# Kernel optimization log

Measured on AMD Instinct MI355X. Metric: run time of the kernel, lower is better.

## Reference

```python
import jax, jax.numpy as jnp
import numpy as np
import math

D_MODEL = 256
N_HEADS = 8
NUM_NODES = 20
KSIZE = 3
EPS = 1e-5


def _ln(x, g, b):
    m = jnp.mean(x, axis=-1, keepdims=True)
    v = jnp.mean(jnp.square(x - m), axis=-1, keepdims=True)
    return (x - m) * jax.lax.rsqrt(v + EPS) * g + b


def _conv1d(x_bdn, w_oik):
    # x: [B, D, N], w: [O, I, K], SAME padding, no bias
    return jax.lax.conv_general_dilated(
        x_bdn, w_oik, window_strides=(1,), padding='SAME',
        dimension_numbers=('NCH', 'OIH', 'NCH'))


def setup_inputs() -> dict:
    key = jax.random.key(0)
    ks = jax.random.split(key, 12)
    B, N, D, H, K = 8192, NUM_NODES, D_MODEL, N_HEADS, KSIZE
    s = 1.0 / math.sqrt(D * K)
    inp = {
        'x': jax.random.normal(ks[0], (B, N, D), jnp.float32),
        'wq': jax.random.normal(ks[1], (D, D, K), jnp.float32) * s,
        'wk': jax.random.normal(ks[2], (D, D, K), jnp.float32) * s,
        'wv': jax.random.normal(ks[3], (D, D, K), jnp.float32) * s,
        'gq': jnp.ones((D,), jnp.float32), 'bq': jnp.zeros((D,), jnp.float32),
        'gk': jnp.ones((D,), jnp.float32), 'bk': jnp.zeros((D,), jnp.float32),
        'gv': jnp.ones((D,), jnp.float32), 'bv': jnp.zeros((D,), jnp.float32),
        'rel_table': jax.random.normal(ks[4], (2 * N - 1, H), jnp.float32) * 0.02,
        'gbias': jax.random.normal(ks[5], (H, N, N), jnp.float32) * 0.02,
        'alpha': jnp.float32(1.0),
        'wo': jax.random.normal(ks[6], (D, D), jnp.float32) * (1.0 / math.sqrt(D)),
        'bo': jnp.zeros((D,), jnp.float32),
    }
    return inp


def reference(x, wq, wk, wv, gq, bq, gk, bk, gv, bv, rel_table, gbias, alpha, wo, bo):
    B, N, D = x.shape
    H = N_HEADS
    dk = D // H
    xp = jnp.transpose(x, (0, 2, 1))  # [B, D, N]
    q = x + _ln(jnp.transpose(_conv1d(xp, wq), (0, 2, 1)), gq, bq)
    k = x + _ln(jnp.transpose(_conv1d(xp, wk), (0, 2, 1)), gk, bk)
    v = x + _ln(jnp.transpose(_conv1d(xp, wv), (0, 2, 1)), gv, bv)
    q = q.reshape(B, N, H, dk).transpose(0, 2, 1, 3)  # [B, H, N, dk]
    k = k.reshape(B, N, H, dk).transpose(0, 2, 1, 3)
    v = v.reshape(B, N, H, dk).transpose(0, 2, 1, 3)
    scores = jnp.einsum('bhnd,bhmd->bhnm', q, k) / math.sqrt(dk)
    # relative position bias: index table [2N-1, H] -> [1, H, N, N]
    coords = jnp.arange(N)
    rel_idx = coords[:, None] - coords[None, :] + N - 1  # [N, N]
    rel_bias = rel_table[rel_idx]  # [N, N, H]
    scores = scores + jnp.transpose(rel_bias, (2, 0, 1))[None]
    scores = scores + gbias[None] * alpha
    attn = jax.nn.softmax(scores, axis=-1)
    out = jnp.einsum('bhnm,bhmd->bhnd', attn, v)  # dropout p=0
    out = out.transpose(0, 2, 1, 3).reshape(B, N, D)
    return out @ wo.T + bo
```

## Files before the change

### kernel.cpp

```cpp
#include <hip/hip_runtime.h>
#include <hip/hip_bf16.h>
#include <stdint.h>

#define BATCH 8192
#define NNODE 20
#define MROWS 163840
#define KCONV 768
#define NCONV 768

typedef __bf16 bf16x8 __attribute__((ext_vector_type(8)));
typedef float f32x4 __attribute__((ext_vector_type(4)));
typedef unsigned short u16x4 __attribute__((ext_vector_type(4)));
typedef unsigned short u16x8 __attribute__((ext_vector_type(8)));

#define GLOBAL_AS __attribute__((address_space(1)))
#define LDS_AS __attribute__((address_space(3)))

__device__ __forceinline__ void load_lds16(const void* g, void* l) {
  __builtin_amdgcn_global_load_lds((const GLOBAL_AS uint32_t*)g,
                                   (LDS_AS uint32_t*)l, 16, 0, 0);
}

__device__ __forceinline__ float bf2f(unsigned short u) {
  union { unsigned int i; float f; } x;
  x.i = ((unsigned int)u) << 16;
  return x.f;
}

__global__ void prep_kernel(const float* __restrict__ x,
                            const float* __restrict__ wq,
                            const float* __restrict__ wk,
                            const float* __restrict__ wv,
                            const float* __restrict__ wo,
                            __hip_bfloat16* __restrict__ xb,
                            __hip_bfloat16* __restrict__ WcT,
                            __hip_bfloat16* __restrict__ wob,
                            int* __restrict__ zrow) {
  const int stride = gridDim.x * blockDim.x;
  const int gid = blockIdx.x * blockDim.x + threadIdx.x;

  if (gid < 128) zrow[gid] = 0;

  const int n8 = (MROWS * 256) / 8;
  for (int i8 = gid; i8 < n8; i8 += stride) {
    const float4* xp = ((const float4*)x) + (size_t)i8 * 2;
    float4 a = xp[0];
    float4 b = xp[1];
    __align__(16) __hip_bfloat16 h[8];
    h[0] = __float2bfloat16(a.x); h[1] = __float2bfloat16(a.y);
    h[2] = __float2bfloat16(a.z); h[3] = __float2bfloat16(a.w);
    h[4] = __float2bfloat16(b.x); h[5] = __float2bfloat16(b.y);
    h[6] = __float2bfloat16(b.z); h[7] = __float2bfloat16(b.w);
    ((int4*)xb)[i8] = *(const int4*)h;
  }

  for (int idx = gid; idx < NCONV * KCONV; idx += stride) {
    int n = idx / KCONV;
    int j = idx - n * KCONV;
    int c = n >> 8, o = n & 255;
    int t = j >> 8, i = j & 255;
    const float* w = (c == 0) ? wq : (c == 1) ? wk : wv;
    WcT[idx] = __float2bfloat16(w[(o * 256 + i) * 3 + t]);
  }

  for (int idx = gid; idx < 256 * 256; idx += stride) {
    wob[idx] = __float2bfloat16(wo[idx]);
  }
}

__global__ __launch_bounds__(256) void conv_gemm_kernel(
    const __hip_bfloat16* __restrict__ xb,
    const __hip_bfloat16* __restrict__ WcT,
    __hip_bfloat16* __restrict__ y,
    const __hip_bfloat16* __restrict__ zrow) {
  __shared__ __align__(16) __hip_bfloat16 As[128 * 64];
  __shared__ __align__(16) __hip_bfloat16 Bs[128 * 64];

  const int tid = threadIdx.x;
  const int lane = tid & 63;
  const int wave = tid >> 6;
  const int wm = (wave >> 1) << 6;
  const int wn = (wave & 1) << 6;
  const int l16 = lane & 15;
  const int quad = lane >> 4;
  const int m0 = blockIdx.x * 128;
  const int n0 = blockIdx.y * 128;

  const __hip_bfloat16* a_base[4];
  const __hip_bfloat16* z_base[4];
  const __hip_bfloat16* b_base[4];
  int a_node[4];
  int lds_off[4];
#pragma unroll
  for (int it = 0; it < 4; ++it) {
    int flat = ((it * 4 + wave) << 6) + lane;
    int row = flat >> 3;
    int seg = flat & 7;
    int seg_g = seg ^ (row & 7);
    int gr = m0 + row;
    int b = gr / 20;
    int node = gr - b * 20;
    a_node[it] = node;
    a_base[it] = xb + (long)(gr - 1) * 256 + seg_g * 8;
    z_base[it] = zrow + seg_g * 8;
    b_base[it] = WcT + (size_t)(n0 + row) * KCONV + seg_g * 8;
    lds_off[it] = (it * 4 + wave) << 9;
  }

  f32x4 acc[4][4];
  const f32x4 zero = {0.f, 0.f, 0.f, 0.f};
#pragma unroll
  for (int i = 0; i < 4; ++i)
#pragma unroll
    for (int j = 0; j < 4; ++j) acc[i][j] = zero;

  for (int kt = 0; kt < 12; ++kt) {
    const int t = kt >> 2;
    const int i0 = (kt & 3) << 6;
    const int k0 = kt << 6;
#pragma unroll
    for (int it = 0; it < 4; ++it) {
      bool ok = (unsigned)(a_node[it] + t - 1) < 20u;
      const __hip_bfloat16* ga = ok ? (a_base[it] + t * 256 + i0) : z_base[it];
      load_lds16(ga, &As[lds_off[it]]);
      load_lds16(b_base[it] + k0, &Bs[lds_off[it]]);
    }
    __syncthreads();

#pragma unroll
    for (int kk = 0; kk < 64; kk += 32) {
      const int sx = (((kk >> 3) + quad) ^ (l16 & 7)) << 3;
      bf16x8 af[4], bfr[4];
#pragma unroll
      for (int i = 0; i < 4; ++i)
        af[i] = *(const bf16x8*)&As[((wm + i * 16 + l16) << 6) + sx];
#pragma unroll
      for (int j = 0; j < 4; ++j)
        bfr[j] = *(const bf16x8*)&Bs[((wn + j * 16 + l16) << 6) + sx];
#pragma unroll
      for (int i = 0; i < 4; ++i)
#pragma unroll
        for (int j = 0; j < 4; ++j)
          acc[i][j] = __builtin_amdgcn_mfma_f32_16x16x32_bf16(af[i], bfr[j],
                                                              acc[i][j], 0, 0, 0);
    }
    __syncthreads();
  }

#pragma unroll
  for (int i = 0; i < 4; ++i)
#pragma unroll
    for (int j = 0; j < 4; ++j)
#pragma unroll
      for (int r = 0; r < 4; ++r) {
        int row = m0 + wm + i * 16 + quad * 4 + r;
        int col = n0 + wn + j * 16 + l16;
        y[(size_t)row * NCONV + col] = __float2bfloat16(acc[i][j][r]);
      }
}

#define YST 776
__global__ __launch_bounds__(256) void attn2_kernel(
    const __hip_bfloat16* __restrict__ y,
    const __hip_bfloat16* __restrict__ xb,
    const float* __restrict__ rel,
    const float* __restrict__ gbias,
    const float* __restrict__ alpha_p,
    const float* __restrict__ gq, const float* __restrict__ bq,
    const float* __restrict__ gk, const float* __restrict__ bk,
    const float* __restrict__ gv, const float* __restrict__ bv,
    __hip_bfloat16* __restrict__ ao) {
  __shared__ __align__(16) __hip_bfloat16 yS[20 * YST];
  __shared__ float scS[8 * 20 * 20];

  const int b = blockIdx.x;
  const int tid = threadIdx.x;
  const float alpha = alpha_p[0];

  const int4* src4 = (const int4*)(y + (size_t)b * NNODE * 768);
#pragma unroll
  for (int p = 0; p < 8; ++p) {
    int idx = tid + p * 256;
    if (idx < 1920) {
      int r = idx / 96;
      int c = idx - r * 96;
      *(int4*)&yS[r * YST + c * 8] = src4[idx];
    }
  }
  __syncthreads();

  if (tid < 240) {
    const int rc = tid >> 2;
    const int p = tid & 3;
    const int r = rc / 3;
    const int c = rc - r * 3;
    unsigned short* lp = (unsigned short*)&yS[r * YST + c * 256 + p * 64];

    float sum = 0.f, sq = 0.f;
#pragma unroll
    for (int s = 0; s < 8; ++s) {
      u16x8 v = *(const u16x8*)&lp[s * 8];
#pragma unroll
      for (int e = 0; e < 8; ++e) {
        float t = bf2f(v[e]);
        sum += t;
        sq += t * t;
      }
    }
    sum += __shfl_xor(sum, 1, 64); sq += __shfl_xor(sq, 1, 64);
    sum += __shfl_xor(sum, 2, 64); sq += __shfl_xor(sq, 2, 64);

    const float mean = sum * (1.0f / 256.0f);
    const float var = sq * (1.0f / 256.0f) - mean * mean;
    const float rstd = rsqrtf(var + 1e-5f);

    const float* g = (c == 0) ? gq : (c == 1) ? gk : gv;
    const float* bb = (c == 0) ? bq : (c == 1) ? bk : bv;
    const unsigned short* xp =
        (const unsigned short*)&xb[(((size_t)b * NNODE + r) << 8) + p * 64];

#pragma unroll
    for (int s = 0; s < 8; ++s) {
      u16x8 v = *(const u16x8*)&lp[s * 8];
      u16x8 xv = *(const u16x8*)&xp[s * 8];
      float4 g0 = *(const float4*)&g[p * 64 + s * 8];
      float4 g1 = *(const float4*)&g[p * 64 + s * 8 + 4];
      float4 b0 = *(const float4*)&bb[p * 64 + s * 8];
      float4 b1 = *(const float4*)&bb[p * 64 + s * 8 + 4];
      const float* gf0 = (const float*)&g0;
      const float* gf1 = (const float*)&g1;
      const float* bf0 = (const float*)&b0;
      const float* bf1 = (const float*)&b1;
      __align__(16) __hip_bfloat16 h[8];
#pragma unroll
      for (int e = 0; e < 4; ++e)
        h[e] = __float2bfloat16(bf2f(xv[e]) +
                                (bf2f(v[e]) - mean) * rstd * gf0[e] + bf0[e]);
#pragma unroll
      for (int e = 0; e < 4; ++e)
        h[4 + e] = __float2bfloat16(bf2f(xv[4 + e]) +
                                    (bf2f(v[4 + e]) - mean) * rstd * gf1[e] +
                                    bf1[e]);
      *(int4*)&lp[s * 8] = *(const int4*)h;
    }
  }
  __syncthreads();

#pragma unroll
  for (int p = 0; p < 4; ++p) {
    int flat = tid + p * 256;
    if (flat < 800) {
      int h = flat / 100;
      int rem = flat - h * 100;
      int i = rem / 5;
      int j0 = (rem - i * 5) * 4;
      const unsigned short* qp = (const unsigned short*)&yS[i * YST + h * 32];
      float qf[32];
#pragma unroll
      for (int d = 0; d < 32; ++d) qf[d] = bf2f(qp[d]);
      float4 gb4 = *(const float4*)&gbias[h * 400 + i * 20 + j0];
#pragma unroll
      for (int jj = 0; jj < 4; ++jj) {
        int j = j0 + jj;
        const unsigned short* kp = (const unsigned short*)&yS[j * YST + 256 + h * 32];
        float dot = 0.f;
#pragma unroll
        for (int d = 0; d < 32; ++d) dot += qf[d] * bf2f(kp[d]);
        scS[h * 400 + i * 20 + j] = dot * 0.17677669529663687f +
                                    rel[(i - j + 19) * 8 + h] +
                                    ((const float*)&gb4)[jj] * alpha;
      }
    }
  }
  __syncthreads();

  if (tid < 160) {
    float* row = scS + tid * 20;
    float mx = row[0];
#pragma unroll
    for (int j = 1; j < 20; ++j) mx = fmaxf(mx, row[j]);
    float s = 0.f;
    float e[20];
#pragma unroll
    for (int j = 0; j < 20; ++j) {
      e[j] = __expf(row[j] - mx);
      s += e[j];
    }
    float inv = 1.0f / s;
#pragma unroll
    for (int j = 0; j < 20; ++j) row[j] = e[j] * inv;
  }
  __syncthreads();

#pragma unroll
  for (int p = 0; p < 5; ++p) {
    int flat = tid + p * 256;
    int col = flat & 255;
    int i0 = (flat >> 8) << 2;
    int h = col >> 5;
    const unsigned short* vp = (const unsigned short*)yS;
    float o[4] = {0.f, 0.f, 0.f, 0.f};
#pragma unroll
    for (int j = 0; j < 20; ++j) {
      float vv = bf2f(vp[j * YST + 512 + col]);
#pragma unroll
      for (int ii = 0; ii < 4; ++ii)
        o[ii] += scS[h * 400 + (i0 + ii) * 20 + j] * vv;
    }
#pragma unroll
    for (int ii = 0; ii < 4; ++ii)
      ao[(((size_t)(b * NNODE + i0 + ii)) << 8) + col] = __float2bfloat16(o[ii]);
  }
}

__global__ __launch_bounds__(256) void proj_gemm_kernel(
    const __hip_bfloat16* __restrict__ ao,
    const __hip_bfloat16* __restrict__ wob,
    const float* __restrict__ bo,
    float* __restrict__ out) {
  __shared__ __align__(16) __hip_bfloat16 As[128 * 64];
  __shared__ __align__(16) __hip_bfloat16 Bs[128 * 64];

  const int tid = threadIdx.x;
  const int lane = tid & 63;
  const int wave = tid >> 6;
  const int wm = (wave >> 1) << 6;
  const int wn = (wave & 1) << 6;
  const int l16 = lane & 15;
  const int quad = lane >> 4;
  const int m0 = blockIdx.x * 128;
  const int n0 = blockIdx.y * 128;

  const __hip_bfloat16* a_base[4];
  const __hip_bfloat16* b_base[4];
  int lds_off[4];
#pragma unroll
  for (int it = 0; it < 4; ++it) {
    int flat = ((it * 4 + wave) << 6) + lane;
    int row = flat >> 3;
    int seg = flat & 7;
    int seg_g = seg ^ (row & 7);
    a_base[it] = ao + (((size_t)(m0 + row)) << 8) + seg_g * 8;
    b_base[it] = wob + (((size_t)(n0 + row)) << 8) + seg_g * 8;
    lds_off[it] = (it * 4 + wave) << 9;
  }

  f32x4 acc[4][4];
  const f32x4 zero = {0.f, 0.f, 0.f, 0.f};
#pragma unroll
  for (int i = 0; i < 4; ++i)
#pragma unroll
    for (int j = 0; j < 4; ++j) acc[i][j] = zero;

  for (int kt = 0; kt < 4; ++kt) {
    const int k0 = kt << 6;
#pragma unroll
    for (int it = 0; it < 4; ++it) {
      load_lds16(a_base[it] + k0, &As[lds_off[it]]);
      load_lds16(b_base[it] + k0, &Bs[lds_off[it]]);
    }
    __syncthreads();

#pragma unroll
    for (int kk = 0; kk < 64; kk += 32) {
      const int sx = (((kk >> 3) + quad) ^ (l16 & 7)) << 3;
      bf16x8 af[4], bfr[4];
#pragma unroll
      for (int i = 0; i < 4; ++i)
        af[i] = *(const bf16x8*)&As[((wm + i * 16 + l16) << 6) + sx];
#pragma unroll
      for (int j = 0; j < 4; ++j)
        bfr[j] = *(const bf16x8*)&Bs[((wn + j * 16 + l16) << 6) + sx];
#pragma unroll
      for (int i = 0; i < 4; ++i)
#pragma unroll
        for (int j = 0; j < 4; ++j)
          acc[i][j] = __builtin_amdgcn_mfma_f32_16x16x32_bf16(af[i], bfr[j],
                                                              acc[i][j], 0, 0, 0);
    }
    __syncthreads();
  }

#pragma unroll
  for (int i = 0; i < 4; ++i)
#pragma unroll
    for (int j = 0; j < 4; ++j) {
      int col = n0 + wn + j * 16 + l16;
      float bias = bo[col];
#pragma unroll
      for (int r = 0; r < 4; ++r) {
        int row = m0 + wm + i * 16 + quad * 4 + r;
        out[(size_t)row * 256 + col] = acc[i][j][r] + bias;
      }
    }
}

extern "C" void kernel_launch(void* const* d_in, const int* in_sizes, int n_in,
                              void* d_out, int out_size, void* d_ws, size_t ws_size,
                              hipStream_t stream) {
  const float* x     = (const float*)d_in[0];
  const float* wq    = (const float*)d_in[1];
  const float* wk    = (const float*)d_in[2];
  const float* wv    = (const float*)d_in[3];
  const float* gq    = (const float*)d_in[4];
  const float* bq    = (const float*)d_in[5];
  const float* gk    = (const float*)d_in[6];
  const float* bk    = (const float*)d_in[7];
  const float* gv    = (const float*)d_in[8];
  const float* bv    = (const float*)d_in[9];
  const float* rel   = (const float*)d_in[10];
  const float* gbias = (const float*)d_in[11];
  const float* alpha = (const float*)d_in[12];
  const float* wo    = (const float*)d_in[13];
  const float* bo    = (const float*)d_in[14];
  float* out = (float*)d_out;

  char* ws = (char*)d_ws;
  __hip_bfloat16* xb  = (__hip_bfloat16*)(ws);
  __hip_bfloat16* y   = (__hip_bfloat16*)(ws + 83886080);
  __hip_bfloat16* ao  = (__hip_bfloat16*)(ws + 335544320);
  __hip_bfloat16* WcT = (__hip_bfloat16*)(ws + 419430400);
  __hip_bfloat16* wob = (__hip_bfloat16*)(ws + 420610048);
  int*            zr  = (int*)(ws + 420741120);

  prep_kernel<<<8192, 256, 0, stream>>>(x, wq, wk, wv, wo, xb, WcT, wob, zr);
  conv_gemm_kernel<<<dim3(1280, 6), 256, 0, stream>>>(xb, WcT, y,
                                                      (const __hip_bfloat16*)zr);
  attn2_kernel<<<8192, 256, 0, stream>>>(y, xb, rel, gbias, alpha,
                                         gq, bq, gk, bk, gv, bv, ao);
  proj_gemm_kernel<<<dim3(1280, 2), 256, 0, stream>>>(ao, wob, bo, out);
}
```

Baseline: 857.6 us.

## Use MFMA for attention QK^T and PV with precomputed bias and prefetched residual

Replaces the scalar per-thread dot products for attention scores and the attention-times-V product with bf16 MFMA 16x16x32 instructions per head. Probabilities are written as bf16 into a zero-padded LDS tile and V is transposed into LDS. The relative and global bias is precomputed into the score buffer before the QK stage, and residual x loads are issued early so they overlap the tile load. Adds LDS usage and rounds softmax probabilities to bf16, which may reduce occupancy slightly and change numerics.

```diff
diff --git a/kernel.cpp b/kernel.cpp
--- a/kernel.cpp
+++ b/kernel.cpp
@@ -160,7 +160,7 @@
 }
 
 #define YST 776
-__global__ __launch_bounds__(256) void attn2_kernel(
+__global__ __launch_bounds__(256) void attn3_kernel(
     const __hip_bfloat16* __restrict__ y,
     const __hip_bfloat16* __restrict__ xb,
     const float* __restrict__ rel,
@@ -171,11 +171,17 @@
     const float* __restrict__ gv, const float* __restrict__ bv,
     __hip_bfloat16* __restrict__ ao) {
   __shared__ __align__(16) __hip_bfloat16 yS[20 * YST];
-  __shared__ float scS[8 * 20 * 20];
+  __shared__ __align__(16) float scS[8 * 400];
+  __shared__ __align__(16) __hip_bfloat16 pS[8 * 32 * 32];
+  __shared__ __align__(16) __hip_bfloat16 vT[8 * 32 * 32];
 
   const int b = blockIdx.x;
   const int tid = threadIdx.x;
   const float alpha = alpha_p[0];
+  const int lane = tid & 63;
+  const int wave = tid >> 6;
+  const int l16 = lane & 15;
+  const int quad = lane >> 4;
 
   const int4* src4 = (const int4*)(y + (size_t)b * NNODE * 768);
 #pragma unroll
@@ -187,6 +193,40 @@
       *(int4*)&yS[r * YST + c * 8] = src4[idx];
     }
   }
+  {
+    const int4 z4 = {0, 0, 0, 0};
+#pragma unroll
+    for (int p = 0; p < 4; ++p) ((int4*)pS)[tid + p * 256] = z4;
+#pragma unroll
+    for (int p = 0; p < 4; ++p) ((int4*)vT)[tid + p * 256] = z4;
+  }
+#pragma unroll
+  for (int p = 0; p < 4; ++p) {
+    int idx = tid + p * 256;
+    if (idx < 800) {
+      int h = idx / 100;
+      int rem = idx - h * 100;
+      int i = rem / 5;
+      int j0 = (rem - i * 5) * 4;
+      float4 gb = ((const float4*)gbias)[idx];
+      float4 o;
+      o.x = gb.x * alpha + rel[(i - j0 + 19) * 8 + h];
+      o.y = gb.y * alpha + rel[(i - j0 + 18) * 8 + h];
+      o.z = gb.z * alpha + rel[(i - j0 + 17) * 8 + h];
+      o.w = gb.w * alpha + rel[(i - j0 + 16) * 8 + h];
+      *(float4*)&scS[idx * 4] = o;
+    }
+  }
+  u16x8 xr[8];
+  if (tid < 240) {
+    const int rc = tid >> 2;
+    const int p = tid & 3;
+    const int r = rc / 3;
+    const unsigned short* xp =
+        (const unsigned short*)&xb[(((size_t)b * NNODE + r) << 8) + p * 64];
+#pragma unroll
+    for (int s = 0; s < 8; ++s) xr[s] = *(const u16x8*)&xp[s * 8];
+  }
   __syncthreads();
 
   if (tid < 240) {
@@ -216,13 +256,11 @@
 
     const float* g = (c == 0) ? gq : (c == 1) ? gk : gv;
     const float* bb = (c == 0) ? bq : (c == 1) ? bk : bv;
-    const unsigned short* xp =
-        (const unsigned short*)&xb[(((size_t)b * NNODE + r) << 8) + p * 64];
 
 #pragma unroll
     for (int s = 0; s < 8; ++s) {
       u16x8 v = *(const u16x8*)&lp[s * 8];
-      u16x8 xv = *(const u16x8*)&xp[s * 8];
+      u16x8 xv = xr[s];
       float4 g0 = *(const float4*)&g[p * 64 + s * 8];
       float4 g1 = *(const float4*)&g[p * 64 + s * 8 + 4];
       float4 b0 = *(const float4*)&bb[p * 64 + s * 8];
@@ -246,70 +284,105 @@
   }
   __syncthreads();
 
-#pragma unroll
-  for (int p = 0; p < 4; ++p) {
-    int flat = tid + p * 256;
-    if (flat < 800) {
-      int h = flat / 100;
-      int rem = flat - h * 100;
-      int i = rem / 5;
-      int j0 = (rem - i * 5) * 4;
-      const unsigned short* qp = (const unsigned short*)&yS[i * YST + h * 32];
-      float qf[32];
-#pragma unroll
-      for (int d = 0; d < 32; ++d) qf[d] = bf2f(qp[d]);
-      float4 gb4 = *(const float4*)&gbias[h * 400 + i * 20 + j0];
-#pragma unroll
-      for (int jj = 0; jj < 4; ++jj) {
-        int j = j0 + jj;
-        const unsigned short* kp = (const unsigned short*)&yS[j * YST + 256 + h * 32];
-        float dot = 0.f;
-#pragma unroll
-        for (int d = 0; d < 32; ++d) dot += qf[d] * bf2f(kp[d]);
-        scS[h * 400 + i * 20 + j] = dot * 0.17677669529663687f +
-                                    rel[(i - j + 19) * 8 + h] +
-                                    ((const float*)&gb4)[jj] * alpha;
+  {
+    const int h = tid >> 5, dk = tid & 31;
+    const unsigned short* vcol = (const unsigned short*)yS + 512 + h * 32 + dk;
+    __align__(16) unsigned short tmp[20];
+#pragma unroll
+    for (int r = 0; r < 20; ++r) tmp[r] = vcol[r * YST];
+    unsigned short* dst = (unsigned short*)&vT[(h * 32 + dk) * 32];
+    *(int4*)&dst[0] = *(const int4*)&tmp[0];
+    *(int4*)&dst[8] = *(const int4*)&tmp[8];
+    *(int2*)&dst[16] = *(const int2*)&tmp[16];
+  }
+  {
+    const int rA0 = l16;
+    const int rA1 = (l16 + 16 < 20) ? (l16 + 16) : 19;
+    const float scale = 0.17677669529663687f;
+    const f32x4 zero = {0.f, 0.f, 0.f, 0.f};
+#pragma unroll
+    for (int hh = 0; hh < 2; ++hh) {
+      const int h = wave * 2 + hh;
+      bf16x8 a0 = *(const bf16x8*)&yS[rA0 * YST + h * 32 + quad * 8];
+      bf16x8 a1 = *(const bf16x8*)&yS[rA1 * YST + h * 32 + quad * 8];
+      bf16x8 b0 = *(const bf16x8*)&yS[rA0 * YST + 256 + h * 32 + quad * 8];
+      bf16x8 b1 = *(const bf16x8*)&yS[rA1 * YST + 256 + h * 32 + quad * 8];
+      f32x4 c00 = __builtin_amdgcn_mfma_f32_16x16x32_bf16(a0, b0, zero, 0, 0, 0);
+      f32x4 c01 = __builtin_amdgcn_mfma_f32_16x16x32_bf16(a0, b1, zero, 0, 0, 0);
+      f32x4 c10 = __builtin_amdgcn_mfma_f32_16x16x32_bf16(a1, b0, zero, 0, 0, 0);
+      f32x4 c11 = __builtin_amdgcn_mfma_f32_16x16x32_bf16(a1, b1, zero, 0, 0, 0);
+      float* srow = scS + h * 400;
+#pragma unroll
+      for (int r = 0; r < 4; ++r) {
+        const int i0 = quad * 4 + r;
+        srow[i0 * 20 + l16] += c00[r] * scale;
+        if (l16 < 4) srow[i0 * 20 + 16 + l16] += c01[r] * scale;
+        const int iB = 16 + i0;
+        if (iB < 20) {
+          srow[iB * 20 + l16] += c10[r] * scale;
+          if (l16 < 4) srow[iB * 20 + 16 + l16] += c11[r] * scale;
+        }
       }
     }
   }
   __syncthreads();
 
   if (tid < 160) {
-    float* row = scS + tid * 20;
+    const int h = tid / 20;
+    const int i = tid - h * 20;
+    const float* row = scS + h * 400 + i * 20;
     float mx = row[0];
 #pragma unroll
     for (int j = 1; j < 20; ++j) mx = fmaxf(mx, row[j]);
+    float e[20];
     float s = 0.f;
-    float e[20];
 #pragma unroll
     for (int j = 0; j < 20; ++j) {
       e[j] = __expf(row[j] - mx);
       s += e[j];
     }
-    float inv = 1.0f / s;
-#pragma unroll
-    for (int j = 0; j < 20; ++j) row[j] = e[j] * inv;
+    const float inv = 1.0f / s;
+    __align__(16) __hip_bfloat16 hb[32];
+#pragma unroll
+    for (int j = 0; j < 20; ++j) hb[j] = __float2bfloat16(e[j] * inv);
+#pragma unroll
+    for (int j = 20; j < 32; ++j) hb[j] = __float2bfloat16(0.f);
+    __hip_bfloat16* dst = &pS[(h * 32 + i) * 32];
+#pragma unroll
+    for (int q = 0; q < 4; ++q)
+      ((int4*)dst)[q] = ((const int4*)hb)[q];
   }
   __syncthreads();
 
-#pragma unroll
-  for (int p = 0; p < 5; ++p) {
-    int flat = tid + p * 256;
-    int col = flat & 255;
-    int i0 = (flat >> 8) << 2;
-    int h = col >> 5;
-    const unsigned short* vp = (const unsigned short*)yS;
-    float o[4] = {0.f, 0.f, 0.f, 0.f};
-#pragma unroll
-    for (int j = 0; j < 20; ++j) {
-      float vv = bf2f(vp[j * YST + 512 + col]);
-#pragma unroll
-      for (int ii = 0; ii < 4; ++ii)
-        o[ii] += scS[h * 400 + (i0 + ii) * 20 + j] * vv;
-    }
-#pragma unroll
-    for (int ii = 0; ii < 4; ++ii)
-      ao[(((size_t)(b * NNODE + i0 + ii)) << 8) + col] = __float2bfloat16(o[ii]);
+  {
+    const f32x4 zero = {0.f, 0.f, 0.f, 0.f};
+#pragma unroll
+    for (int hh = 0; hh < 2; ++hh) {
+      const int h = wave * 2 + hh;
+      bf16x8 a0 = *(const bf16x8*)&pS[(h * 32 + l16) * 32 + quad * 8];
+      bf16x8 a1 = *(const bf16x8*)&pS[(h * 32 + 16 + l16) * 32 + quad * 8];
+      bf16x8 b0 = *(const bf16x8*)&vT[(h * 32 + l16) * 32 + quad * 8];
+      bf16x8 b1 = *(const bf16x8*)&vT[(h * 32 + 16 + l16) * 32 + quad * 8];
+      f32x4 c00 = __builtin_amdgcn_mfma_f32_16x16x32_bf16(a0, b0, zero, 0, 0, 0);
+      f32x4 c01 = __builtin_amdgcn_mfma_f32_16x16x32_bf16(a0, b1, zero, 0, 0, 0);
+      f32x4 c10 = __builtin_amdgcn_mfma_f32_16x16x32_bf16(a1, b0, zero, 0, 0, 0);
+      f32x4 c11 = __builtin_amdgcn_mfma_f32_16x16x32_bf16(a1, b1, zero, 0, 0, 0);
+#pragma unroll
+      for (int r = 0; r < 4; ++r) {
+        const int i0 = quad * 4 + r;
+        ao[(((size_t)(b * 20 + i0)) << 8) + h * 32 + l16] =
+            __float2bfloat16(c00[r]);
+        ao[(((size_t)(b * 20 + i0)) << 8) + h * 32 + 16 + l16] =
+            __float2bfloat16(c01[r]);
+        const int iB = 16 + i0;
+        if (iB < 20) {
+          ao[(((size_t)(b * 20 + iB)) << 8) + h * 32 + l16] =
+              __float2bfloat16(c10[r]);
+          ao[(((size_t)(b * 20 + iB)) << 8) + h * 32 + 16 + l16] =
+              __float2bfloat16(c11[r]);
+        }
+      }
+    }
   }
 }
 
@@ -426,7 +499,7 @@
   prep_kernel<<<8192, 256, 0, stream>>>(x, wq, wk, wv, wo, xb, WcT, wob, zr);
   conv_gemm_kernel<<<dim3(1280, 6), 256, 0, stream>>>(xb, WcT, y,
                                                       (const __hip_bfloat16*)zr);
-  attn2_kernel<<<8192, 256, 0, stream>>>(y, xb, rel, gbias, alpha,
+  attn3_kernel<<<8192, 256, 0, stream>>>(y, xb, rel, gbias, alpha,
                                          gq, bq, gk, bk, gv, bv, ao);
   proj_gemm_kernel<<<dim3(1280, 2), 256, 0, stream>>>(ao, wob, bo, out);
 }
```

Measured after the change: 861.2 us. No clear change (+0.4%).

## Compute attention scores and PV with MFMA in registers, drop score LDS buffer

Applied to the files above, without the earlier changes.

Replaces the scalar QK dot products, LDS score buffer, and scalar softmax/PV loops with per-wave MFMA 16x16x32 bf16 ops. Softmax now runs in registers with cross-lane shuffles, and probabilities are repacked into MFMA operands via shuffles. The 1/sqrt(dk) scale is folded into Q during the LayerNorm pass, x is prefetched into registers before the first barrier, and the LN column mapping is interleaved for better LDS access. This removes two barriers and most of the scalar LDS traffic, at the cost of padding 20x20 tiles to 32x32 and rounding probabilities to bf16.

```diff
diff --git a/kernel.cpp b/kernel.cpp
--- a/kernel.cpp
+++ b/kernel.cpp
@@ -7,10 +7,10 @@
 #define MROWS 163840
 #define KCONV 768
 #define NCONV 768
+#define QSCALE 0.17677669529663687f
 
 typedef __bf16 bf16x8 __attribute__((ext_vector_type(8)));
 typedef float f32x4 __attribute__((ext_vector_type(4)));
-typedef unsigned short u16x4 __attribute__((ext_vector_type(4)));
 typedef unsigned short u16x8 __attribute__((ext_vector_type(8)));
 
 #define GLOBAL_AS __attribute__((address_space(1)))
@@ -160,7 +160,7 @@
 }
 
 #define YST 776
-__global__ __launch_bounds__(256) void attn2_kernel(
+__global__ __launch_bounds__(256) void attn5_kernel(
     const __hip_bfloat16* __restrict__ y,
     const __hip_bfloat16* __restrict__ xb,
     const float* __restrict__ rel,
@@ -171,11 +171,15 @@
     const float* __restrict__ gv, const float* __restrict__ bv,
     __hip_bfloat16* __restrict__ ao) {
   __shared__ __align__(16) __hip_bfloat16 yS[20 * YST];
-  __shared__ float scS[8 * 20 * 20];
 
   const int b = blockIdx.x;
   const int tid = threadIdx.x;
   const float alpha = alpha_p[0];
+  const int lane = tid & 63;
+  const int wave = tid >> 6;
+  const int l16 = lane & 15;
+  const int quad = lane >> 4;
+  const f32x4 zero = {0.f, 0.f, 0.f, 0.f};
 
   const int4* src4 = (const int4*)(y + (size_t)b * NNODE * 768);
 #pragma unroll
@@ -187,6 +191,16 @@
       *(int4*)&yS[r * YST + c * 8] = src4[idx];
     }
   }
+  u16x8 xr[8];
+  if (tid < 240) {
+    const int rc = tid >> 2;
+    const int p = tid & 3;
+    const int r = rc / 3;
+    const unsigned short* xp =
+        (const unsigned short*)&xb[(((size_t)b * NNODE + r)) << 8];
+#pragma unroll
+    for (int s = 0; s < 8; ++s) xr[s] = *(const u16x8*)&xp[(s * 4 + p) * 8];
+  }
   __syncthreads();
 
   if (tid < 240) {
@@ -194,12 +208,12 @@
     const int p = tid & 3;
     const int r = rc / 3;
     const int c = rc - r * 3;
-    unsigned short* lp = (unsigned short*)&yS[r * YST + c * 256 + p * 64];
+    unsigned short* lp = (unsigned short*)&yS[r * YST + c * 256];
 
     float sum = 0.f, sq = 0.f;
 #pragma unroll
     for (int s = 0; s < 8; ++s) {
-      u16x8 v = *(const u16x8*)&lp[s * 8];
+      u16x8 v = *(const u16x8*)&lp[(s * 4 + p) * 8];
 #pragma unroll
       for (int e = 0; e < 8; ++e) {
         float t = bf2f(v[e]);
@@ -213,20 +227,20 @@
     const float mean = sum * (1.0f / 256.0f);
     const float var = sq * (1.0f / 256.0f) - mean * mean;
     const float rstd = rsqrtf(var + 1e-5f);
+    const float osc = (c == 0) ? QSCALE : 1.0f;
 
     const float* g = (c == 0) ? gq : (c == 1) ? gk : gv;
     const float* bb = (c == 0) ? bq : (c == 1) ? bk : bv;
-    const unsigned short* xp =
-        (const unsigned short*)&xb[(((size_t)b * NNODE + r) << 8) + p * 64];
 
 #pragma unroll
     for (int s = 0; s < 8; ++s) {
-      u16x8 v = *(const u16x8*)&lp[s * 8];
-      u16x8 xv = *(const u16x8*)&xp[s * 8];
-      float4 g0 = *(const float4*)&g[p * 64 + s * 8];
-      float4 g1 = *(const float4*)&g[p * 64 + s * 8 + 4];
-      float4 b0 = *(const float4*)&bb[p * 64 + s * 8];
-      float4 b1 = *(const float4*)&bb[p * 64 + s * 8 + 4];
+      const int c0 = (s * 4 + p) * 8;
+      u16x8 v = *(const u16x8*)&lp[c0];
+      u16x8 xv = xr[s];
+      float4 g0 = *(const float4*)&g[c0];
+      float4 g1 = *(const float4*)&g[c0 + 4];
+      float4 b0 = *(const float4*)&bb[c0];
+      float4 b1 = *(const float4*)&bb[c0 + 4];
       const float* gf0 = (const float*)&g0;
       const float* gf1 = (const float*)&g1;
       const float* bf0 = (const float*)&b0;
@@ -234,82 +248,143 @@
       __align__(16) __hip_bfloat16 h[8];
 #pragma unroll
       for (int e = 0; e < 4; ++e)
-        h[e] = __float2bfloat16(bf2f(xv[e]) +
-                                (bf2f(v[e]) - mean) * rstd * gf0[e] + bf0[e]);
+        h[e] = __float2bfloat16(
+            (bf2f(xv[e]) + (bf2f(v[e]) - mean) * rstd * gf0[e] + bf0[e]) * osc);
 #pragma unroll
       for (int e = 0; e < 4; ++e)
-        h[4 + e] = __float2bfloat16(bf2f(xv[4 + e]) +
-                                    (bf2f(v[4 + e]) - mean) * rstd * gf1[e] +
-                                    bf1[e]);
-      *(int4*)&lp[s * 8] = *(const int4*)h;
+        h[4 + e] = __float2bfloat16(
+            (bf2f(xv[4 + e]) + (bf2f(v[4 + e]) - mean) * rstd * gf1[e] + bf1[e]) * osc);
+      *(int4*)&lp[c0] = *(const int4*)h;
     }
   }
   __syncthreads();
 
-#pragma unroll
-  for (int p = 0; p < 4; ++p) {
-    int flat = tid + p * 256;
-    if (flat < 800) {
-      int h = flat / 100;
-      int rem = flat - h * 100;
-      int i = rem / 5;
-      int j0 = (rem - i * 5) * 4;
-      const unsigned short* qp = (const unsigned short*)&yS[i * YST + h * 32];
-      float qf[32];
-#pragma unroll
-      for (int d = 0; d < 32; ++d) qf[d] = bf2f(qp[d]);
-      float4 gb4 = *(const float4*)&gbias[h * 400 + i * 20 + j0];
-#pragma unroll
-      for (int jj = 0; jj < 4; ++jj) {
-        int j = j0 + jj;
-        const unsigned short* kp = (const unsigned short*)&yS[j * YST + 256 + h * 32];
-        float dot = 0.f;
-#pragma unroll
-        for (int d = 0; d < 32; ++d) dot += qf[d] * bf2f(kp[d]);
-        scS[h * 400 + i * 20 + j] = dot * 0.17677669529663687f +
-                                    rel[(i - j + 19) * 8 + h] +
-                                    ((const float*)&gb4)[jj] * alpha;
-      }
-    }
-  }
-  __syncthreads();
-
-  if (tid < 160) {
-    float* row = scS + tid * 20;
-    float mx = row[0];
-#pragma unroll
-    for (int j = 1; j < 20; ++j) mx = fmaxf(mx, row[j]);
-    float s = 0.f;
-    float e[20];
-#pragma unroll
-    for (int j = 0; j < 20; ++j) {
-      e[j] = __expf(row[j] - mx);
-      s += e[j];
-    }
-    float inv = 1.0f / s;
-#pragma unroll
-    for (int j = 0; j < 20; ++j) row[j] = e[j] * inv;
-  }
-  __syncthreads();
-
-#pragma unroll
-  for (int p = 0; p < 5; ++p) {
-    int flat = tid + p * 256;
-    int col = flat & 255;
-    int i0 = (flat >> 8) << 2;
-    int h = col >> 5;
-    const unsigned short* vp = (const unsigned short*)yS;
-    float o[4] = {0.f, 0.f, 0.f, 0.f};
-#pragma unroll
-    for (int j = 0; j < 20; ++j) {
-      float vv = bf2f(vp[j * YST + 512 + col]);
-#pragma unroll
-      for (int ii = 0; ii < 4; ++ii)
-        o[ii] += scS[h * 400 + (i0 + ii) * 20 + j] * vv;
-    }
-#pragma unroll
-    for (int ii = 0; ii < 4; ++ii)
-      ao[(((size_t)(b * NNODE + i0 + ii)) << 8) + col] = __float2bfloat16(o[ii]);
+  const unsigned short* ySu = (const unsigned short*)yS;
+#pragma unroll
+  for (int hh = 0; hh < 2; ++hh) {
+    const int h = wave * 2 + hh;
+    const int rlo = l16;
+    const int rhi = (l16 + 16 < 20) ? (l16 + 16) : 19;
+
+    bf16x8 kf0 = *(const bf16x8*)&yS[rlo * YST + 256 + h * 32 + quad * 8];
+    bf16x8 kf1 = *(const bf16x8*)&yS[rhi * YST + 256 + h * 32 + quad * 8];
+    bf16x8 qf0 = *(const bf16x8*)&yS[rlo * YST + h * 32 + quad * 8];
+    bf16x8 qf1 = *(const bf16x8*)&yS[rhi * YST + h * 32 + quad * 8];
+
+    f32x4 c00, c01, c10, c11;
+    {
+      const float4 g00 = *(const float4*)&gbias[h * 400 + rlo * 20 + quad * 4];
+      const float4 g01 = *(const float4*)&gbias[h * 400 + rhi * 20 + quad * 4];
+#pragma unroll
+      for (int r = 0; r < 4; ++r) {
+        const int j0 = quad * 4 + r;
+        const int j1 = (16 + j0 < 20) ? (16 + j0) : 19;
+        c00[r] = alpha * ((const float*)&g00)[r] + rel[(rlo - j0 + 19) * 8 + h];
+        c01[r] = alpha * ((const float*)&g01)[r] + rel[(rhi - j0 + 19) * 8 + h];
+        c10[r] = alpha * gbias[h * 400 + rlo * 20 + j1] + rel[(rlo - j1 + 19) * 8 + h];
+        c11[r] = alpha * gbias[h * 400 + rhi * 20 + j1] + rel[(rhi - j1 + 19) * 8 + h];
+      }
+    }
+    c00 = __builtin_amdgcn_mfma_f32_16x16x32_bf16(kf0, qf0, c00, 0, 0, 0);
+    c01 = __builtin_amdgcn_mfma_f32_16x16x32_bf16(kf0, qf1, c01, 0, 0, 0);
+    c10 = __builtin_amdgcn_mfma_f32_16x16x32_bf16(kf1, qf0, c10, 0, 0, 0);
+    c11 = __builtin_amdgcn_mfma_f32_16x16x32_bf16(kf1, qf1, c11, 0, 0, 0);
+
+    float p00[4], p10[4], p01[4], p11[4];
+    {
+      float m = fmaxf(fmaxf(c00[0], c00[1]), fmaxf(c00[2], c00[3]));
+      if (quad == 0)
+        m = fmaxf(m, fmaxf(fmaxf(c10[0], c10[1]), fmaxf(c10[2], c10[3])));
+      m = fmaxf(m, __shfl_xor(m, 16, 64));
+      m = fmaxf(m, __shfl_xor(m, 32, 64));
+      float s = 0.f;
+#pragma unroll
+      for (int r = 0; r < 4; ++r) { p00[r] = __expf(c00[r] - m); s += p00[r]; }
+#pragma unroll
+      for (int r = 0; r < 4; ++r) {
+        p10[r] = (quad == 0) ? __expf(c10[r] - m) : 0.f;
+        s += p10[r];
+      }
+      s += __shfl_xor(s, 16, 64);
+      s += __shfl_xor(s, 32, 64);
+      const float inv = 1.0f / s;
+#pragma unroll
+      for (int r = 0; r < 4; ++r) { p00[r] *= inv; p10[r] *= inv; }
+    }
+    {
+      float m = fmaxf(fmaxf(c01[0], c01[1]), fmaxf(c01[2], c01[3]));
+      if (quad == 0)
+        m = fmaxf(m, fmaxf(fmaxf(c11[0], c11[1]), fmaxf(c11[2], c11[3])));
+      m = fmaxf(m, __shfl_xor(m, 16, 64));
+      m = fmaxf(m, __shfl_xor(m, 32, 64));
+      float s = 0.f;
+#pragma unroll
+      for (int r = 0; r < 4; ++r) { p01[r] = __expf(c01[r] - m); s += p01[r]; }
+#pragma unroll
+      for (int r = 0; r < 4; ++r) {
+        p11[r] = (quad == 0) ? __expf(c11[r] - m) : 0.f;
+        s += p11[r];
+      }
+      s += __shfl_xor(s, 16, 64);
+      s += __shfl_xor(s, 32, 64);
+      const float inv = 1.0f / s;
+#pragma unroll
+      for (int r = 0; r < 4; ++r) { p01[r] *= inv; p11[r] *= inv; }
+    }
+
+    const int srcA = ((quad * 2) & 3) * 16 + l16;
+    const int srcB = ((quad * 2 + 1) & 3) * 16 + l16;
+    __align__(16) __hip_bfloat16 aLo[8], aHi[8];
+#pragma unroll
+    for (int r = 0; r < 4; ++r) {
+      float xa = __shfl(p00[r], srcA, 64);
+      float xc = __shfl(p00[r], srcB, 64);
+      float xt = __shfl(p10[r], l16, 64);
+      float lo = (quad < 2) ? xa : ((quad == 2) ? xt : 0.f);
+      float hi = (quad < 2) ? xc : 0.f;
+      aLo[r] = __float2bfloat16(lo);
+      aLo[4 + r] = __float2bfloat16(hi);
+      float ya = __shfl(p01[r], srcA, 64);
+      float yc = __shfl(p01[r], srcB, 64);
+      float yt = __shfl(p11[r], l16, 64);
+      lo = (quad < 2) ? ya : ((quad == 2) ? yt : 0.f);
+      hi = (quad < 2) ? yc : 0.f;
+      aHi[r] = __float2bfloat16(lo);
+      aHi[4 + r] = __float2bfloat16(hi);
+    }
+
+    __align__(16) __hip_bfloat16 bv0[8], bv1[8];
+#pragma unroll
+    for (int e = 0; e < 8; ++e) {
+      int jj = quad * 8 + e;
+      int jc = (jj < 20) ? jj : 19;
+      const __hip_bfloat16* vp =
+          (const __hip_bfloat16*)&ySu[jc * YST + 512 + h * 32];
+      bv0[e] = vp[l16];
+      bv1[e] = vp[16 + l16];
+    }
+
+    f32x4 d00 = __builtin_amdgcn_mfma_f32_16x16x32_bf16(
+        *(const bf16x8*)aLo, *(const bf16x8*)bv0, zero, 0, 0, 0);
+    f32x4 d01 = __builtin_amdgcn_mfma_f32_16x16x32_bf16(
+        *(const bf16x8*)aLo, *(const bf16x8*)bv1, zero, 0, 0, 0);
+    f32x4 d10 = __builtin_amdgcn_mfma_f32_16x16x32_bf16(
+        *(const bf16x8*)aHi, *(const bf16x8*)bv0, zero, 0, 0, 0);
+    f32x4 d11 = __builtin_amdgcn_mfma_f32_16x16x32_bf16(
+        *(const bf16x8*)aHi, *(const bf16x8*)bv1, zero, 0, 0, 0);
+
+    __hip_bfloat16* aob = ao + (((size_t)(b * 20)) << 8) + h * 32;
+#pragma unroll
+    for (int r = 0; r < 4; ++r) {
+      const int i0 = quad * 4 + r;
+      aob[i0 * 256 + l16] = __float2bfloat16(d00[r]);
+      aob[i0 * 256 + 16 + l16] = __float2bfloat16(d01[r]);
+      const int i1 = 16 + i0;
+      if (i1 < 20) {
+        aob[i1 * 256 + l16] = __float2bfloat16(d10[r]);
+        aob[i1 * 256 + 16 + l16] = __float2bfloat16(d11[r]);
+      }
+    }
   }
 }
 
@@ -426,7 +501,7 @@
   prep_kernel<<<8192, 256, 0, stream>>>(x, wq, wk, wv, wo, xb, WcT, wob, zr);
   conv_gemm_kernel<<<dim3(1280, 6), 256, 0, stream>>>(xb, WcT, y,
                                                       (const __hip_bfloat16*)zr);
-  attn2_kernel<<<8192, 256, 0, stream>>>(y, xb, rel, gbias, alpha,
+  attn5_kernel<<<8192, 256, 0, stream>>>(y, xb, rel, gbias, alpha,
                                          gq, bq, gk, bk, gv, bv, ao);
   proj_gemm_kernel<<<dim3(1280, 2), 256, 0, stream>>>(ao, wob, bo, out);
 }
```

Result: faster. 817.4 us (-4.7%).
